# Kernel optimization log

Hardware: AMD Instinct MI355X
Metric: run time of the kernel (lower is better)

The kernel has to match this reference:

```python
import jax, jax.numpy as jnp
import numpy as np

# RootMLP architecture constants (data_size=16, width=64, depth=2, in=1, out=2*data)
DATA = 16
WIDTH = 64
OUT = 2 * DATA
LAYER_SHAPES = [(WIDTH, 1), (WIDTH,), (WIDTH, WIDTH), (WIDTH,), (OUT, WIDTH), (OUT,)]
SIZES = [int(np.prod(s)) for s in LAYER_SHAPES]
OFFS = np.cumsum([0] + SIZES).tolist()
LATENT = OFFS[-1]  # 6368


def _mlp_apply(thet, x):
    # Unflatten latent vector into MLP weights (order: W0,b0,W1,b1,W2,b2) and run it.
    W0 = thet[OFFS[0]:OFFS[1]].reshape(WIDTH, 1)
    b0 = thet[OFFS[1]:OFFS[2]]
    W1 = thet[OFFS[2]:OFFS[3]].reshape(WIDTH, WIDTH)
    b1 = thet[OFFS[3]:OFFS[4]]
    W2 = thet[OFFS[4]:OFFS[5]].reshape(OUT, WIDTH)
    b2 = thet[OFFS[5]:OFFS[6]]
    h = jax.nn.relu(W0 @ x + b0)
    h = jax.nn.relu(W1 @ h + b1)
    return W2 @ h + b2  # (OUT,)


def setup_inputs() -> dict:
    key = jax.random.key(0)
    k1, k2, k3, k4 = jax.random.split(key, 4)
    batch, T = 8, 64
    xs = jax.random.normal(k1, (batch, T, DATA), dtype=jnp.float32)
    ts = jnp.tile(jnp.linspace(0.0, 1.0, T, dtype=jnp.float32), (batch, 1))
    # A initialized as identity in the source; tiny noise keeps the recurrence non-trivial yet stable.
    A = jnp.eye(LATENT, dtype=jnp.float32) + 1e-4 * jax.random.normal(k2, (LATENT, LATENT), dtype=jnp.float32)
    B = 0.01 * jax.random.normal(k3, (LATENT, DATA + 1), dtype=jnp.float32)
    theta0 = 0.05 * jax.random.normal(k4, (LATENT,), dtype=jnp.float32)
    return {"xs": xs, "ts": ts, "A": A, "B": B, "theta0": theta0}


def reference(xs, ts, A, B, theta0):
    # xs: (batch, T, DATA); ts: (batch, T)
    def forward(xs_, ts_):
        def f(carry, inp):
            thet, x_hat, x_prev, t_prev = carry
            x_true, t_curr = inp  # x_true: (DATA,), t_curr: (1,)
            delta_t = t_curr - t_prev
            # forcing_prob = 1.0  ->  bernoulli(key, 1.0) is always True -> teacher forcing
            x_t = x_true
            # time_as_channel=True: prepend time to both current and previous inputs
            xt_c = jnp.concatenate([t_curr, x_t])
            xp_c = jnp.concatenate([t_prev, x_prev])
            thet_next = A @ thet + B @ (xt_c - xp_c)
            root_in = t_curr + delta_t  # (1,)
            out = _mlp_apply(thet_next, root_in)  # (2*DATA,)
            mean = jnp.tanh(out[:DATA])
            std = jax.nn.softplus(jnp.tanh(out[DATA:]))  # apply_tanh_uncertainty=True
            x_next = jnp.concatenate([mean, std])
            # carry update per source: new x_hat = mean, new x_prev = old x_hat
            return (thet_next, mean, x_hat, t_curr), x_next

        init = (theta0, xs_[0], xs_[0], -ts_[1:2])
        _, ys = jax.lax.scan(f, init, (xs_, ts_[:, None]))
        return ys  # (T, 2*DATA)

    return jax.vmap(forward)(xs, ts)
```

## Files before the change

### kernel.cpp

```cpp
#include <hip/hip_runtime.h>
#include <hip/hip_bf16.h>
#include <cmath>

#define LATENT 6368
#define TSTEPS 64
#define NDATA 16
#define NPANEL 398
#define KSPLIT 8
#define NCHUNK 199
#define CPS 25
#define NTILE (NPANEL*KSPLIT)
#define KBLK 796
#define AGENT __HIP_MEMORY_SCOPE_AGENT
#define TSTR  51200
#define TTSTR 102400

typedef __attribute__((ext_vector_type(8))) short short8v;
typedef __attribute__((ext_vector_type(4))) float floatx4;

__device__ __forceinline__ unsigned short f2bf(float x) {
    union { float f; unsigned u; } c; c.f = x;
    unsigned r = (c.u + 0x7FFFu + ((c.u >> 16) & 1u)) >> 16;
    return (unsigned short)r;
}
__device__ __forceinline__ float bf2f(unsigned short h) {
    union { unsigned u; float f; } c; c.u = ((unsigned)h) << 16; return c.f;
}

__device__ __forceinline__ void stfc(float* p, float v) {
    __hip_atomic_store(p, v, __ATOMIC_RELAXED, AGENT);
}
__device__ __forceinline__ void stu16c(unsigned short* p, unsigned short v) {
    __hip_atomic_store(p, v, __ATOMIC_RELAXED, AGENT);
}

__global__ __launch_bounds__(64) void row_scale(const float* __restrict__ A,
                                                float* __restrict__ S) {
    int row = blockIdx.x;
    int lane = threadIdx.x;
    const float* Ar = A + (size_t)row * LATENT;
    float m = 0.f;
    for (int i = 0; i < 25; ++i) {
        int idx = i * 256 + lane * 4;
        if (idx + 4 <= LATENT) {
            float4 v = *reinterpret_cast<const float4*>(Ar + idx);
            float a0 = v.x - (idx + 0 == row ? 1.f : 0.f);
            float a1 = v.y - (idx + 1 == row ? 1.f : 0.f);
            float a2 = v.z - (idx + 2 == row ? 1.f : 0.f);
            float a3 = v.w - (idx + 3 == row ? 1.f : 0.f);
            m = fmaxf(m, fmaxf(fmaxf(fabsf(a0), fabsf(a1)), fmaxf(fabsf(a2), fabsf(a3))));
        }
    }
#pragma unroll
    for (int o = 32; o; o >>= 1) m = fmaxf(m, __shfl_xor(m, o, 64));
    if (lane == 0) S[row] = fmaxf(m, 1e-30f) * (1.0f / 32767.0f);
}

__global__ __launch_bounds__(256) void convert_Eq(const float* __restrict__ A,
                                                  const float* __restrict__ S,
                                                  short* __restrict__ Eq,
                                                  int total) {
    int t = blockIdx.x * 256 + threadIdx.x;
    if (t >= total) return;
    int row = t / KBLK;
    int kb  = t - row * KBLK;
    const float4* src = reinterpret_cast<const float4*>(A + (size_t)row * LATENT + kb * 8);
    float4 v0 = src[0];
    float4 v1 = src[1];
    float v[8] = {v0.x, v0.y, v0.z, v0.w, v1.x, v1.y, v1.z, v1.w};
    int jd = row - kb * 8;
    if (jd >= 0 && jd < 8) v[jd] -= 1.0f;
    float inv = 1.0f / S[row];
    union { short8v s; short q[8]; } o;
#pragma unroll
    for (int j = 0; j < 8; ++j) {
        float qf = rintf(v[j] * inv);
        qf = fminf(fmaxf(qf, -32767.f), 32767.f);
        o.q[j] = (short)qf;
    }
    int p = row >> 4, rowl = row & 15, c = kb >> 2, kgrp = kb & 3;
    int lane = kgrp * 16 + rowl;
    *reinterpret_cast<short8v*>(Eq + ((size_t)(p * NCHUNK + c)) * 512 + lane * 8) = o.s;
}

__global__ __launch_bounds__(256) void init_theta(const float* __restrict__ th0,
                                                  float* __restrict__ T0,
                                                  unsigned short* __restrict__ TT0) {
    int r = blockIdx.x * blockDim.x + threadIdx.x;
    if (r >= LATENT) return;
    float v = th0[r];
#pragma unroll
    for (int b = 0; b < 8; ++b) T0[r * 8 + b] = v;
    unsigned short hb = f2bf(v);
    unsigned short lb = f2bf(v - bf2f(hb));
    int c = r >> 5, kg = (r & 31) >> 3, j = r & 7;
    size_t base = (size_t)c * 512 + kg * 128;
#pragma unroll
    for (int n = 0; n < 8; ++n) {
        TT0[base + n * 8 + j] = hb;
        TT0[base + (n + 8) * 8 + j] = lb;
    }
}

__device__ void mlp_batch_rot(const float* __restrict__ Tcur, const float* __restrict__ ts,
                              float* __restrict__ mwrite, float* __restrict__ ys,
                              int i, int b, int lane) {
    float tc = ts[b * TSTEPS + i];
    float tp = (i == 0) ? -ts[b * TSTEPS + 1] : ts[b * TSTEPS + i - 1];
    float rin = 2.f * tc - tp;
    float h0 = fmaxf(Tcur[(size_t)lane * 8 + b] * rin + Tcur[(size_t)(64 + lane) * 8 + b], 0.f);
    float h1 = Tcur[(size_t)(4224 + lane) * 8 + b];
#pragma unroll 8
    for (int k = 0; k < 64; ++k)
        h1 += Tcur[(size_t)(128 + lane * 64 + k) * 8 + b] * __shfl(h0, k, 64);
    h1 = fmaxf(h1, 0.f);
    float o = 0.f;
    if (lane < 32) o = Tcur[(size_t)(6336 + lane) * 8 + b];
#pragma unroll 8
    for (int k = 0; k < 64; ++k) {
        float hk = __shfl(h1, k, 64);
        if (lane < 32) o += Tcur[(size_t)(4288 + lane * 64 + k) * 8 + b] * hk;
    }
    if (lane < 32) {
        float z = tanhf(o);
        float res;
        if (lane < 16) { res = z; stfc(&mwrite[b * NDATA + lane], z); }
        else           { res = log1pf(expf(z)); }
        ys[(size_t)b * (TSTEPS * 32) + (size_t)i * 32 + lane] = res;
    }
}

__device__ void mlp_batch(const float* __restrict__ Tcur, const float* __restrict__ ts,
                          float* __restrict__ mwrite, float* __restrict__ ys,
                          int i, int b, int lane) {
    float tc = ts[b * TSTEPS + i];
    float tp = (i == 0) ? -ts[b * TSTEPS + 1] : ts[b * TSTEPS + i - 1];
    float rin = 2.f * tc - tp;
    float h0 = fmaxf(Tcur[(size_t)lane * 8 + b] * rin + Tcur[(size_t)(64 + lane) * 8 + b], 0.f);
    float h1 = Tcur[(size_t)(4224 + lane) * 8 + b];
#pragma unroll 8
    for (int k = 0; k < 64; ++k)
        h1 += Tcur[(size_t)(128 + lane * 64 + k) * 8 + b] * __shfl(h0, k, 64);
    h1 = fmaxf(h1, 0.f);
    float o = 0.f;
    if (lane < 32) o = Tcur[(size_t)(6336 + lane) * 8 + b];
#pragma unroll 8
    for (int k = 0; k < 64; ++k) {
        float hk = __shfl(h1, k, 64);
        if (lane < 32) o += Tcur[(size_t)(4288 + lane * 64 + k) * 8 + b] * hk;
    }
    if (lane < 32) {
        float z = tanhf(o);
        float res;
        if (lane < 16) { res = z; mwrite[b * NDATA + lane] = z; }
        else           { res = log1pf(expf(z)); }
        ys[(size_t)b * (TSTEPS * 32) + (size_t)i * 32 + lane] = res;
    }
}

__device__ __forceinline__ void gsync2(unsigned* grpCnt, unsigned* superCnt,
                                       unsigned* gEpoch, unsigned iter) {
    asm volatile("s_waitcnt vmcnt(0)" ::: "memory");
    __syncthreads();
    if (threadIdx.x == 0) {
        unsigned g = blockIdx.x & 15u;
        unsigned gsz = (g < 8u) ? 13u : 12u;
        unsigned v = __hip_atomic_fetch_add(&grpCnt[g * 32], 1u, __ATOMIC_RELAXED, AGENT);
        if (v == iter * gsz - 1u) {
            unsigned w = __hip_atomic_fetch_add(superCnt, 1u, __ATOMIC_RELAXED, AGENT);
            if (w == iter * 16u - 1u) {
#pragma unroll
                for (int i2 = 0; i2 < 16; ++i2)
                    __hip_atomic_store(&gEpoch[i2 * 32], iter, __ATOMIC_RELAXED, AGENT);
            }
        }
        while (__hip_atomic_load(&gEpoch[g * 32], __ATOMIC_RELAXED, AGENT) < iter)
            __builtin_amdgcn_s_sleep(4);
    }
    __syncthreads();
}

#define COMP2(EA, EB, TP) do {                                                    \
    union { short8v sv; unsigned short us[8]; } HA, LA, HB, LB;                   \
    _Pragma("unroll")                                                             \
    for (int j = 0; j < 8; ++j) {                                                 \
        int qa = (EA)[j], qb = (EB)[j];                                           \
        union { float f; unsigned u; } x0, x1, x2, x3;                            \
        x0.f = (float)(qa >> 8);  HA.us[j] = (unsigned short)(x0.u >> 16);        \
        x1.f = (float)(qa & 255); LA.us[j] = (unsigned short)(x1.u >> 16);        \
        x2.f = (float)(qb >> 8);  HB.us[j] = (unsigned short)(x2.u >> 16);        \
        x3.f = (float)(qb & 255); LB.us[j] = (unsigned short)(x3.u >> 16);        \
    }                                                                             \
    acc1A = __builtin_amdgcn_mfma_f32_16x16x32_bf16(HA.sv, (TP), acc1A, 0, 0, 0); \
    acc2A = __builtin_amdgcn_mfma_f32_16x16x32_bf16(LA.sv, (TP), acc2A, 0, 0, 0); \
    acc1B = __builtin_amdgcn_mfma_f32_16x16x32_bf16(HB.sv, (TP), acc1B, 0, 0, 0); \
    acc2B = __builtin_amdgcn_mfma_f32_16x16x32_bf16(LB.sv, (TP), acc2B, 0, 0, 0); \
} while (0)

#define LDE(P)  (*reinterpret_cast<const short8v*>(P))

__global__ __launch_bounds__(1024, 4) void persistent9(
    const short* __restrict__ Eq, const float* __restrict__ S,
    float* __restrict__ Tbase, unsigned short* __restrict__ TTbase,
    float* __restrict__ mbase,
    const float* __restrict__ Bmat, const float* __restrict__ xs,
    const float* __restrict__ ts, float* __restrict__ ys,
    unsigned* grpCnt, unsigned* superCnt, unsigned* gEpoch)
{
    __shared__ float red[16][2][16][16];
    __shared__ float ush[17][8];
    int tid = threadIdx.x, blk = blockIdx.x;
    int wave = tid >> 6, lane = tid & 63;
    int rowl = lane & 15, kgrp = lane >> 4;
    int cs = (wave < 7) ? wave * 13 : 91 + (wave - 7) * 12;
    int nch = (wave < 7) ? 13 : 12;
    int panelA = blk * 2;
    unsigned iter = 0;
    for (int s = 0; s < TSTEPS; ++s) {
        const float* Tc = Tbase + (size_t)(64 - s) * TSTR;
        float* Tn       = Tbase + (size_t)(63 - s) * TSTR;
        const unsigned short* TTc = TTbase + (size_t)(64 - s) * TTSTR;
        unsigned short* TTn       = TTbase + (size_t)(63 - s) * TTSTR;
        float* mwrite = mbase + (size_t)(64 - s) * 128;
        const float* mread = mbase + (size_t)(65 - s) * 128;
        if (blk < 199) {
            if (tid < 136) {
                int b = tid & 7, j = tid >> 3;
                float tc = ts[b * TSTEPS + s];
                float tp = (s == 0) ? -ts[b * TSTEPS + 1] : ts[b * TSTEPS + s - 1];
                float val;
                if (j == 0) val = tc - tp;
                else {
                    int d = j - 1;
                    float xp = (s < 2) ? xs[(b * TSTEPS) * NDATA + d]
                                       : mread[b * NDATA + d];
                    val = xs[(b * TSTEPS + s) * NDATA + d] - xp;
                }
                ush[j][b] = val;
            }
            floatx4 acc1A = {0.f,0.f,0.f,0.f}, acc2A = {0.f,0.f,0.f,0.f};
            floatx4 acc1B = {0.f,0.f,0.f,0.f}, acc2B = {0.f,0.f,0.f,0.f};
            const short* epA = Eq + ((size_t)(panelA * NCHUNK + cs)) * 512 + lane * 8;
            const short* epB = epA + (size_t)NCHUNK * 512;
            const unsigned short* tq = TTc + (size_t)cs * 512 + lane * 8;
            short8v a0 = LDE(epA),        a1 = LDE(epA + 512),
                    a2 = LDE(epA + 1024), a3 = LDE(epA + 1536);
            short8v b0 = LDE(epB),        b1 = LDE(epB + 512),
                    b2 = LDE(epB + 1024), b3 = LDE(epB + 1536);
            short8v t0 = LDE(tq),         t1 = LDE(tq + 512),
                    t2 = LDE(tq + 1024),  t3 = LDE(tq + 1536);
            int c = 0;
            for (; c + 8 <= nch; c += 4) {
                COMP2(a0, b0, t0); a0 = LDE(epA + 2048); b0 = LDE(epB + 2048); t0 = LDE(tq + 2048);
                COMP2(a1, b1, t1); a1 = LDE(epA + 2560); b1 = LDE(epB + 2560); t1 = LDE(tq + 2560);
                COMP2(a2, b2, t2); a2 = LDE(epA + 3072); b2 = LDE(epB + 3072); t2 = LDE(tq + 3072);
                COMP2(a3, b3, t3); a3 = LDE(epA + 3584); b3 = LDE(epB + 3584); t3 = LDE(tq + 3584);
                epA += 2048; epB += 2048; tq += 2048;
            }
            COMP2(a0, b0, t0); COMP2(a1, b1, t1); COMP2(a2, b2, t2); COMP2(a3, b3, t3);
            for (int k2 = 4; c + k2 < nch; ++k2) {
                a0 = LDE(epA + k2 * 512); b0 = LDE(epB + k2 * 512); t0 = LDE(tq + k2 * 512);
                COMP2(a0, b0, t0);
            }
#pragma unroll
            for (int r = 0; r < 4; ++r) {
                red[wave][0][kgrp * 4 + r][rowl] = 256.f * acc1A[r] + acc2A[r];
                red[wave][1][kgrp * 4 + r][rowl] = 256.f * acc1B[r] + acc2B[r];
            }
            __syncthreads();
            if (tid < 256) {
                int m32 = tid >> 3, n = tid & 7;
                int ph = m32 >> 4, m = m32 & 15;
                float sum = 0.f;
#pragma unroll
                for (int w = 0; w < 16; ++w)
                    sum += red[w][ph][m][n] + red[w][ph][m][n + 8];
                int r = blk * 32 + m32;
                float val = Tc[r * 8 + n] + S[r] * sum;
                const float* Brow = Bmat + r * 17;
#pragma unroll
                for (int j = 0; j < 17; ++j) val += Brow[j] * ush[j][n];
                stfc(&Tn[r * 8 + n], val);
                unsigned short hb = f2bf(val);
                int kg = m32 >> 3, j2 = m32 & 7;
                size_t tb = (size_t)blk * 512 + kg * 128;
                stu16c(&TTn[tb + n * 8 + j2], hb);
                stu16c(&TTn[tb + (n + 8) * 8 + j2], f2bf(val - bf2f(hb)));
            }
        } else {
            if (s >= 1 && wave < 8)
                mlp_batch_rot(Tc, ts, mwrite, ys, s - 1, wave, lane);
        }
        ++iter; gsync2(grpCnt, superCnt, gEpoch, iter);
    }
    if (blk == 199 && wave < 8)
        mlp_batch_rot(Tbase, ts, mbase, ys, TSTEPS - 1, wave, lane);
}

template<bool USE_E>
__global__ __launch_bounds__(128) void partial_kernel(
    const short* __restrict__ Eq, const float* __restrict__ S,
    const float* __restrict__ Af,
    const unsigned short* __restrict__ TTc,
    float* __restrict__ P)
{
    int blk = blockIdx.x;
    int p  = blk >> 3;
    int si = blk & 7;
    int tid = threadIdx.x;
    int wave = tid >> 6;
    int lane = tid & 63;
    int rowl = lane & 15;
    int kgrp = lane >> 4;
    int row = p * 16 + rowl;
    int c0 = si * CPS;
    int c1 = c0 + CPS; if (c1 > NCHUNK) c1 = NCHUNK;
    int nch = c1 - c0;
    int half = (nch + 1) >> 1;
    int csw = c0 + wave * half;
    int cew = csw + half; if (cew > c1) cew = c1;
    floatx4 acc1 = {0.f, 0.f, 0.f, 0.f};
    floatx4 acc2 = {0.f, 0.f, 0.f, 0.f};
    for (int c = csw; c < cew; ++c) {
        int k = c * 32 + kgrp * 8;
        short8v ehf, elf;
        if (USE_E) {
            short8v ev = *reinterpret_cast<const short8v*>(
                Eq + ((size_t)(p * NCHUNK + c)) * 512 + lane * 8);
            union { short8v sv; unsigned short us[8]; } EH, EL;
#pragma unroll
            for (int j = 0; j < 8; ++j) {
                int q = ev[j];
                union { float f; unsigned u; } ch2, cl2;
                ch2.f = (float)(q >> 8);
                cl2.f = (float)(q & 255);
                EH.us[j] = (unsigned short)(ch2.u >> 16);
                EL.us[j] = (unsigned short)(cl2.u >> 16);
            }
            ehf = EH.sv; elf = EL.sv;
        } else {
            const float* ap = Af + (size_t)row * LATENT + k;
            float v[8];
#pragma unroll
            for (int j = 0; j < 8; ++j) v[j] = ap[j];
            int jd = row - k;
            if (jd >= 0 && jd < 8) v[jd] -= 1.0f;
            union { short8v sv; unsigned short us[8]; } ch, cl;
#pragma unroll
            for (int j = 0; j < 8; ++j) {
                unsigned short hb = f2bf(v[j]);
                ch.us[j] = hb;
                cl.us[j] = f2bf(v[j] - bf2f(hb));
            }
            ehf = ch.sv; elf = cl.sv;
        }
        short8v tpf = *reinterpret_cast<const short8v*>(TTc + (size_t)c * 512 + lane * 8);
        acc1 = __builtin_amdgcn_mfma_f32_16x16x32_bf16(ehf, tpf, acc1, 0, 0, 0);
        acc2 = __builtin_amdgcn_mfma_f32_16x16x32_bf16(elf, tpf, acc2, 0, 0, 0);
    }
    __shared__ float red[2][16][16];
#pragma unroll
    for (int r = 0; r < 4; ++r)
        red[wave][kgrp * 4 + r][rowl] = USE_E ? (256.f * acc1[r] + acc2[r])
                                              : (acc1[r] + acc2[r]);
    __syncthreads();
    int nn = tid & 15;
    if (nn < 8) {
        for (int mm = tid >> 4; mm < 16; mm += 8) {
            float s2 = red[0][mm][nn] + red[0][mm][nn + 8]
                     + red[1][mm][nn] + red[1][mm][nn + 8];
            if (USE_E) s2 *= S[p * 16 + mm];
            P[((size_t)(p * 8 + si) * 16 + mm) * 8 + nn] = s2;
        }
    }
}

__global__ __launch_bounds__(256) void combine_kernel(
    const float* __restrict__ P,
    const float* __restrict__ Tcur,
    float* __restrict__ Tnxt,
    unsigned short* __restrict__ TTn,
    const float* __restrict__ Bmat,
    const float* __restrict__ xs,
    const float* __restrict__ ts,
    const float* __restrict__ mread,
    float* __restrict__ mwrite,
    float* __restrict__ ys,
    int s, int do_matvec, int do_mlp)
{
    int tid = threadIdx.x;
    if ((int)blockIdx.x < 199) {
        if (!do_matvec) return;
        __shared__ float u[17][8];
        if (tid < 136) {
            int b = tid & 7;
            int j = tid >> 3;
            float tc = ts[b * TSTEPS + s];
            float tp = (s == 0) ? -ts[b * TSTEPS + 1] : ts[b * TSTEPS + s - 1];
            float val;
            if (j == 0) val = tc - tp;
            else {
                int d = j - 1;
                float xp = (s < 2) ? xs[(b * TSTEPS) * NDATA + d] : mread[b * NDATA + d];
                val = xs[(b * TSTEPS + s) * NDATA + d] - xp;
            }
            u[j][b] = val;
        }
        __syncthreads();
        int idx = blockIdx.x * 256 + tid;
        int r = idx >> 3;
        int n = idx & 7;
        int pp = r >> 4, mm = r & 15;
        const float* Pb = P + ((size_t)pp * 8) * 128 + mm * 8 + n;
        float sum = 0.f;
#pragma unroll
        for (int si = 0; si < KSPLIT; ++si) sum += Pb[si * 128];
        float val = Tcur[r * 8 + n] + sum;
        const float* Brow = Bmat + r * 17;
#pragma unroll
        for (int j = 0; j < 17; ++j) val += Brow[j] * u[j][n];
        Tnxt[r * 8 + n] = val;
        unsigned short hb = f2bf(val);
        int c2 = r >> 5, kg = (r & 31) >> 3, j2 = r & 7;
        size_t tb = (size_t)c2 * 512 + kg * 128;
        TTn[tb + n * 8 + j2] = hb;
        TTn[tb + (n + 8) * 8 + j2] = f2bf(val - bf2f(hb));
    } else {
        if (!do_mlp) return;
        int w = tid >> 6, lane = tid & 63;
        for (int it = 0; it < 2; ++it)
            mlp_batch(Tcur, ts, mwrite, ys, s - 1, w * 2 + it, lane);
    }
}

extern "C" void kernel_launch(void* const* d_in, const int* in_sizes, int n_in,
                              void* d_out, int out_size, void* d_ws, size_t ws_size,
                              hipStream_t stream) {
    const float* xs  = (const float*)d_in[0];
    const float* ts  = (const float*)d_in[1];
    const float* A   = (const float*)d_in[2];
    const float* Bm  = (const float*)d_in[3];
    const float* th0 = (const float*)d_in[4];
    float* ys = (float*)d_out;

    char* ws = (char*)d_ws;
    size_t off = 0;
    auto alloc = [&](size_t bytes) {
        void* p = ws + off;
        off += (bytes + 255) & ~(size_t)255;
        return p;
    };
    float* Tbase = (float*)alloc((size_t)65 * TSTR * sizeof(float));
    unsigned short* TTbase = (unsigned short*)alloc((size_t)65 * TTSTR * 2);
    float* mbase = (float*)alloc((size_t)66 * 128 * sizeof(float));
    float* P  = (float*)alloc((size_t)NTILE * 128 * sizeof(float));
    float* S  = (float*)alloc((size_t)LATENT * sizeof(float));
    unsigned* bar = (unsigned*)alloc(8192);
    unsigned* grpCnt   = bar;
    unsigned* superCnt = bar + 512;
    unsigned* gEpoch   = bar + 544;
    size_t Ebytes = (size_t)NPANEL * NCHUNK * 512 * 2;
    bool useE = (off + Ebytes + 512) <= ws_size;
    short* Eq = nullptr;
    if (useE) {
        Eq = (short*)alloc(Ebytes);
        row_scale<<<dim3(LATENT), dim3(64), 0, stream>>>(A, S);
        int nthr = LATENT * KBLK;
        convert_Eq<<<dim3((nthr + 255) / 256), dim3(256), 0, stream>>>(A, S, Eq, nthr);
    }
    init_theta<<<dim3((LATENT + 255) / 256), dim3(256), 0, stream>>>(
        th0, Tbase + (size_t)64 * TSTR, TTbase + (size_t)64 * TTSTR);

    hipError_t coop = hipErrorUnknown;
    if (useE) {
        hipMemsetAsync(bar, 0, 8192, stream);
        void* kargs[] = {
            (void*)&Eq, (void*)&S, (void*)&Tbase, (void*)&TTbase,
            (void*)&mbase, (void*)&Bm, (void*)&xs,
            (void*)&ts, (void*)&ys, (void*)&grpCnt, (void*)&superCnt, (void*)&gEpoch };
        coop = hipLaunchCooperativeKernel((void*)persistent9,
                                          dim3(200), dim3(1024), kargs, 0, stream);
    }
    if (coop != hipSuccess) {
        float* T[2] = {Tbase + (size_t)64 * TSTR, Tbase + (size_t)63 * TSTR};
        unsigned short* TT[2] = {TTbase + (size_t)64 * TTSTR, TTbase + (size_t)63 * TTSTR};
        for (int s = 0; s <= TSTEPS; ++s) {
            int cur = s & 1, nxt = cur ^ 1;
            float* mwrite = mbase + (s & 1) * 128;
            float* mread  = mbase + ((s & 1) ^ 1) * 128;
            int dmv = (s < TSTEPS) ? 1 : 0;
            int dml = (s >= 1) ? 1 : 0;
            if (dmv) {
                if (useE)
                    partial_kernel<true><<<dim3(NTILE), dim3(128), 0, stream>>>(
                        Eq, S, A, TT[cur], P);
                else
                    partial_kernel<false><<<dim3(NTILE), dim3(128), 0, stream>>>(
                        Eq, S, A, TT[cur], P);
            }
            combine_kernel<<<dim3(200), dim3(256), 0, stream>>>(
                P, T[cur], T[nxt], TT[nxt],
                Bm, xs, ts, mread, mwrite, ys, s, dmv, dml);
        }
    }
    (void)in_sizes; (void)n_in; (void)out_size;
}
```

Baseline: 2.384 ms.

## Alternate chunk traversal direction per step and coalesce theta stores via LDS

The persistent kernel now walks its E and theta chunks in reverse order on odd time steps, so the chunks touched last in one step are read first in the next and are more likely to still be in cache. The per-element 32-bit and 16-bit relaxed atomic stores of the new theta (fp32 and split-bf16 copies) are first staged in shared memory. They are then written out as 64-bit atomic stores by 256 threads. This adds an extra __syncthreads and some shared memory per step, in exchange for better cache locality and fewer, wider global stores.

```diff
diff --git a/kernel.cpp b/kernel.cpp
--- a/kernel.cpp
+++ b/kernel.cpp
@@ -31,6 +31,9 @@
     __hip_atomic_store(p, v, __ATOMIC_RELAXED, AGENT);
 }
 __device__ __forceinline__ void stu16c(unsigned short* p, unsigned short v) {
+    __hip_atomic_store(p, v, __ATOMIC_RELAXED, AGENT);
+}
+__device__ __forceinline__ void stu64c(unsigned long long* p, unsigned long long v) {
     __hip_atomic_store(p, v, __ATOMIC_RELAXED, AGENT);
 }
 
@@ -199,7 +202,7 @@
 
 #define LDE(P)  (*reinterpret_cast<const short8v*>(P))
 
-__global__ __launch_bounds__(1024, 4) void persistent9(
+__global__ __launch_bounds__(1024, 4) void persistent10(
     const short* __restrict__ Eq, const float* __restrict__ S,
     float* __restrict__ Tbase, unsigned short* __restrict__ TTbase,
     float* __restrict__ mbase,
@@ -209,6 +212,8 @@
 {
     __shared__ float red[16][2][16][16];
     __shared__ float ush[17][8];
+    __shared__ float stT[256];
+    __shared__ unsigned short stTT[512];
     int tid = threadIdx.x, blk = blockIdx.x;
     int wave = tid >> 6, lane = tid & 63;
     int rowl = lane & 15, kgrp = lane >> 4;
@@ -231,35 +236,38 @@
                 float val;
                 if (j == 0) val = tc - tp;
                 else {
-                    int d = j - 1;
-                    float xp = (s < 2) ? xs[(b * TSTEPS) * NDATA + d]
-                                       : mread[b * NDATA + d];
-                    val = xs[(b * TSTEPS + s) * NDATA + d] - xp;
+                    int d2 = j - 1;
+                    float xp = (s < 2) ? xs[(b * TSTEPS) * NDATA + d2]
+                                       : mread[b * NDATA + d2];
+                    val = xs[(b * TSTEPS + s) * NDATA + d2] - xp;
                 }
                 ush[j][b] = val;
             }
             floatx4 acc1A = {0.f,0.f,0.f,0.f}, acc2A = {0.f,0.f,0.f,0.f};
             floatx4 acc1B = {0.f,0.f,0.f,0.f}, acc2B = {0.f,0.f,0.f,0.f};
-            const short* epA = Eq + ((size_t)(panelA * NCHUNK + cs)) * 512 + lane * 8;
+            int dir = s & 1;
+            long long d = dir ? -512 : 512;
+            int cbeg = dir ? (cs + nch - 1) : cs;
+            const short* epA = Eq + ((size_t)(panelA * NCHUNK + cbeg)) * 512 + lane * 8;
             const short* epB = epA + (size_t)NCHUNK * 512;
-            const unsigned short* tq = TTc + (size_t)cs * 512 + lane * 8;
-            short8v a0 = LDE(epA),        a1 = LDE(epA + 512),
-                    a2 = LDE(epA + 1024), a3 = LDE(epA + 1536);
-            short8v b0 = LDE(epB),        b1 = LDE(epB + 512),
-                    b2 = LDE(epB + 1024), b3 = LDE(epB + 1536);
-            short8v t0 = LDE(tq),         t1 = LDE(tq + 512),
-                    t2 = LDE(tq + 1024),  t3 = LDE(tq + 1536);
+            const unsigned short* tq = TTc + (size_t)cbeg * 512 + lane * 8;
+            short8v a0 = LDE(epA),         a1 = LDE(epA + d),
+                    a2 = LDE(epA + 2 * d), a3 = LDE(epA + 3 * d);
+            short8v b0 = LDE(epB),         b1 = LDE(epB + d),
+                    b2 = LDE(epB + 2 * d), b3 = LDE(epB + 3 * d);
+            short8v t0 = LDE(tq),          t1 = LDE(tq + d),
+                    t2 = LDE(tq + 2 * d),  t3 = LDE(tq + 3 * d);
             int c = 0;
             for (; c + 8 <= nch; c += 4) {
-                COMP2(a0, b0, t0); a0 = LDE(epA + 2048); b0 = LDE(epB + 2048); t0 = LDE(tq + 2048);
-                COMP2(a1, b1, t1); a1 = LDE(epA + 2560); b1 = LDE(epB + 2560); t1 = LDE(tq + 2560);
-                COMP2(a2, b2, t2); a2 = LDE(epA + 3072); b2 = LDE(epB + 3072); t2 = LDE(tq + 3072);
-                COMP2(a3, b3, t3); a3 = LDE(epA + 3584); b3 = LDE(epB + 3584); t3 = LDE(tq + 3584);
-                epA += 2048; epB += 2048; tq += 2048;
+                COMP2(a0, b0, t0); a0 = LDE(epA + 4 * d); b0 = LDE(epB + 4 * d); t0 = LDE(tq + 4 * d);
+                COMP2(a1, b1, t1); a1 = LDE(epA + 5 * d); b1 = LDE(epB + 5 * d); t1 = LDE(tq + 5 * d);
+                COMP2(a2, b2, t2); a2 = LDE(epA + 6 * d); b2 = LDE(epB + 6 * d); t2 = LDE(tq + 6 * d);
+                COMP2(a3, b3, t3); a3 = LDE(epA + 7 * d); b3 = LDE(epB + 7 * d); t3 = LDE(tq + 7 * d);
+                epA += 4 * d; epB += 4 * d; tq += 4 * d;
             }
             COMP2(a0, b0, t0); COMP2(a1, b1, t1); COMP2(a2, b2, t2); COMP2(a3, b3, t3);
             for (int k2 = 4; c + k2 < nch; ++k2) {
-                a0 = LDE(epA + k2 * 512); b0 = LDE(epB + k2 * 512); t0 = LDE(tq + k2 * 512);
+                a0 = LDE(epA + k2 * d); b0 = LDE(epB + k2 * d); t0 = LDE(tq + k2 * d);
                 COMP2(a0, b0, t0);
             }
 #pragma unroll
@@ -280,12 +288,20 @@
                 const float* Brow = Bmat + r * 17;
 #pragma unroll
                 for (int j = 0; j < 17; ++j) val += Brow[j] * ush[j][n];
-                stfc(&Tn[r * 8 + n], val);
+                stT[m32 * 8 + n] = val;
                 unsigned short hb = f2bf(val);
                 int kg = m32 >> 3, j2 = m32 & 7;
-                size_t tb = (size_t)blk * 512 + kg * 128;
-                stu16c(&TTn[tb + n * 8 + j2], hb);
-                stu16c(&TTn[tb + (n + 8) * 8 + j2], f2bf(val - bf2f(hb)));
+                stTT[kg * 128 + n * 8 + j2] = hb;
+                stTT[kg * 128 + (n + 8) * 8 + j2] = f2bf(val - bf2f(hb));
+            }
+            __syncthreads();
+            if (tid < 128) {
+                unsigned long long* dst = (unsigned long long*)(TTn + (size_t)blk * 512);
+                stu64c(&dst[tid], ((const unsigned long long*)stTT)[tid]);
+            } else if (tid < 256) {
+                int t2i = tid - 128;
+                unsigned long long* dst = (unsigned long long*)(Tn + (size_t)blk * 256);
+                stu64c(&dst[t2i], ((const unsigned long long*)stT)[t2i]);
             }
         } else {
             if (s >= 1 && wave < 8)
@@ -478,7 +494,7 @@
             (void*)&Eq, (void*)&S, (void*)&Tbase, (void*)&TTbase,
             (void*)&mbase, (void*)&Bm, (void*)&xs,
             (void*)&ts, (void*)&ys, (void*)&grpCnt, (void*)&superCnt, (void*)&gEpoch };
-        coop = hipLaunchCooperativeKernel((void*)persistent9,
+        coop = hipLaunchCooperativeKernel((void*)persistent10,
                                           dim3(200), dim3(1024), kargs, 0, stream);
     }
     if (coop != hipSuccess) {
```

New measurement: 2.433 ms. 1.02x slower.
